# Kernel tuning notes

Hardware: AMD Instinct MI355X
Metric: run time of the kernel (lower is better)

## Reference

```python
import jax, jax.numpy as jnp
import numpy as np

OUT = 8192   # out_features
IN = 8192    # in_features
GS = 64      # HQQ group_size (axis=0 grouping)
NG = OUT * IN // GS   # number of quantization groups = 1048576
B = 64       # tokens in the batch


def setup_inputs() -> dict:
    key = jax.random.key(0)
    k1, k2, k3, k4, k5 = jax.random.split(key, 5)
    x = jax.random.normal(k1, (B, IN), dtype=jnp.float32)
    # packed 4-bit weights: two 4-bit values per byte, packed along axis 0
    # (HQQ pack_4bit_u8: packed = (W[:GS//2] << 4) | W[GS//2:])
    W_q = jax.random.randint(k2, (GS // 2, NG), 0, 256, dtype=jnp.int32)
    scale = jax.random.uniform(k3, (1, NG), dtype=jnp.float32, minval=0.001, maxval=0.02)
    zero = jax.random.uniform(k4, (1, NG), dtype=jnp.float32, minval=0.0, maxval=15.0)
    bias = jax.random.normal(k5, (OUT,), dtype=jnp.float32) * 0.01
    return {"x": x, "W_q": W_q, "scale": scale, "zero": zero, "bias": bias}


def reference(x, W_q, scale, zero, bias):
    # Unpack 4-bit: high nibble holds rows [0, GS//2), low nibble rows [GS//2, GS)
    hi = (W_q >> 4).astype(jnp.float32)          # (GS//2, NG)
    lo = (W_q & 0xF).astype(jnp.float32)         # (GS//2, NG)
    Wu = jnp.concatenate([hi, lo], axis=0)       # (GS, NG)
    # HQQ group-wise dequant: W = (W_q - zero) * scale, then reshape to (out, in)
    W = ((Wu - zero) * scale).reshape(OUT, IN)
    # linear: y = x @ W^T + bias
    return x @ W.T + bias
```

## Files before the change

### kernel.cpp

```cpp
#include <hip/hip_runtime.h>
#include <stdint.h>

#define OUT_F 8192
#define IN_F  8192
#define NGRP  1048576
#define BATCH 64
#define KS    2
#define NSTEP ((IN_F / KS) / 128)

typedef float f32x4 __attribute__((ext_vector_type(4)));
typedef _Float16 half8_t __attribute__((ext_vector_type(8)));

static __device__ __forceinline__ unsigned int pk_fma_f16(unsigned int a, unsigned int b, unsigned int c) {
  unsigned int d;
  asm("v_pk_fma_f16 %0, %1, %2, %3" : "=v"(d) : "v"(a), "v"(b), "v"(c));
  return d;
}
static __device__ __forceinline__ unsigned int pk16(float a, float b) {
  unsigned short ua = __builtin_bit_cast(unsigned short, (_Float16)a);
  unsigned short ub = __builtin_bit_cast(unsigned short, (_Float16)b);
  return (unsigned int)ua | ((unsigned int)ub << 16);
}

#define GLL16(g, l)                                                         \
  __builtin_amdgcn_global_load_lds(                                         \
      (const __attribute__((address_space(1))) void*)(g),                   \
      (__attribute__((address_space(3))) void*)(l), 16, 0, 0)

__global__ __launch_bounds__(256) void pre_kernel(const float* __restrict__ x, ushort* __restrict__ xh,
                                                  const float* __restrict__ scale, const float* __restrict__ zero,
                                                  uint32_t* __restrict__ szb) {
  const int b = blockIdx.x;
  if (b < 512) {
    const int i = b * 256 + threadIdx.x;
    float4 v = ((const float4*)x)[i];
    ushort4 o;
    o.x = __builtin_bit_cast(unsigned short, (_Float16)v.x);
    o.y = __builtin_bit_cast(unsigned short, (_Float16)v.y);
    o.z = __builtin_bit_cast(unsigned short, (_Float16)v.z);
    o.w = __builtin_bit_cast(unsigned short, (_Float16)v.w);
    ((ushort4*)xh)[i] = o;
  } else {
    const int i = (b - 512) * 256 + threadIdx.x;
    float4 s = ((const float4*)scale)[i];
    float4 z = ((const float4*)zero)[i];
    uint4 o;
    o.x = pk16(s.x, s.y);
    o.y = pk16(-(64.f + z.x) * s.x, -(64.f + z.y) * s.y);
    o.z = pk16(s.z, s.w);
    o.w = pk16(-(64.f + z.z) * s.z, -(64.f + z.w) * s.w);
    ((uint4*)szb)[i] = o;
  }
}

__global__ __launch_bounds__(256, 2) void hqq_gemm_kernel(
    const int* __restrict__ Wq, const uint32_t* __restrict__ szb,
    const ushort* __restrict__ xh, float* __restrict__ part)
{
  __shared__ ushort xlds[3][64 * 128];
  __shared__ ushort blds[2][32 * 128];

  const int t    = threadIdx.x;
  const int bid  = blockIdx.x;
  const int ks   = bid & 1;
  const int gq   = (bid >> 1) & 1;
  const int c    = bid >> 2;
  const int lane = t & 63;
  const int wid  = t >> 6;
  const int kbase = ks * (IN_F / KS);

  const int sr  = t >> 4;
  const int skq = t & 15;
  const int* __restrict__ wqp =
      Wq + (size_t)(gq * 16 + sr) * NGRP + (size_t)c * IN_F + kbase + skq * 8;
  const uint8_t* __restrict__ szp =
      (const uint8_t*)szb + ((size_t)c * IN_F + kbase + skq * 8) * 4;
  const int wbyte = (skq * 16) ^ ((sr & 7) << 4);

  const int tr    = lane & 15;
  const int koff8 = (lane >> 4) * 8;
  const int am    = wid * 16 + tr;

  f32x4 acc_h = {0.f, 0.f, 0.f, 0.f};
  f32x4 acc_l = {0.f, 0.f, 0.f, 0.f};

  auto stage_x = [&](int bi, int s) {
    #pragma unroll
    for (int j = 0; j < 4; ++j) {
      const int m    = wid * 16 + j * 4 + (lane >> 4);
      const int bcol = (lane & 15) * 16;
      const int scol = bcol ^ ((m & 7) << 4);
      const ushort* g = xh + (size_t)m * IN_F + kbase + s * 128 + (scol >> 1);
      ushort* l = &xlds[bi][(wid * 16 + j * 4) * 128];
      GLL16(g, l);
    }
  };

  auto ldregs = [&](int s, int4& wa, int4& wb, uint4& sa, uint4& sb) {
    wa = *(const int4*)(wqp + (size_t)s * 128);
    wb = *(const int4*)(wqp + (size_t)s * 128 + 4);
    sa = *(const uint4*)(szp + (size_t)s * 512);
    sb = *(const uint4*)(szp + (size_t)s * 512 + 16);
  };

  auto stage_b = [&](int bi, const int4& wa, const int4& wb, const uint4& sa, const uint4& sb) {
    uint8_t* bb = (uint8_t*)&blds[bi][0];
    uint4 hi4, lo4;
    {
      unsigned tt = ((unsigned)wa.y << 16) | (unsigned)wa.x;
      hi4.x = pk_fma_f16((tt & 0x00F000F0u) | 0x54005400u, sa.x, sa.y);
      lo4.x = pk_fma_f16(((tt << 4) & 0x00F000F0u) | 0x54005400u, sa.x, sa.y);
    }
    {
      unsigned tt = ((unsigned)wa.w << 16) | (unsigned)wa.z;
      hi4.y = pk_fma_f16((tt & 0x00F000F0u) | 0x54005400u, sa.z, sa.w);
      lo4.y = pk_fma_f16(((tt << 4) & 0x00F000F0u) | 0x54005400u, sa.z, sa.w);
    }
    {
      unsigned tt = ((unsigned)wb.y << 16) | (unsigned)wb.x;
      hi4.z = pk_fma_f16((tt & 0x00F000F0u) | 0x54005400u, sb.x, sb.y);
      lo4.z = pk_fma_f16(((tt << 4) & 0x00F000F0u) | 0x54005400u, sb.x, sb.y);
    }
    {
      unsigned tt = ((unsigned)wb.w << 16) | (unsigned)wb.z;
      hi4.w = pk_fma_f16((tt & 0x00F000F0u) | 0x54005400u, sb.z, sb.w);
      lo4.w = pk_fma_f16(((tt << 4) & 0x00F000F0u) | 0x54005400u, sb.z, sb.w);
    }
    *(uint4*)(bb + sr * 256 + wbyte)        = hi4;
    *(uint4*)(bb + (sr + 16) * 256 + wbyte) = lo4;
  };

  {
    int4 wa0, wb0; uint4 sa0, sb0;
    ldregs(0, wa0, wb0, sa0, sb0);
    stage_b(0, wa0, wb0, sa0, sb0);
  }
  stage_x(0, 0);
  stage_x(1, 1);
  int4 wa, wb; uint4 sa, sb;
  ldregs(1, wa, wb, sa, sb);

  int xr0 = 0, xr1 = 1, xr2 = 2;

  #pragma unroll 1
  for (int s = 0; s < NSTEP; ++s) {
    asm volatile("s_waitcnt lgkmcnt(0)" ::: "memory");
    __builtin_amdgcn_s_barrier();

    const bool more2 = (s + 2 < NSTEP);
    int4 nwa, nwb; uint4 nsa, nsb;
    if (more2) {
      stage_x(xr2, s + 2);
      ldregs(s + 2, nwa, nwb, nsa, nsb);
    }

    if (more2)               asm volatile("s_waitcnt vmcnt(16)" ::: "memory");
    else if (s + 1 < NSTEP)  asm volatile("s_waitcnt vmcnt(8)" ::: "memory");
    else                     asm volatile("s_waitcnt vmcnt(0)" ::: "memory");
    __builtin_amdgcn_sched_barrier(0);

    const uint8_t* xb = (const uint8_t*)&xlds[xr0][0];
    const uint8_t* bb = (const uint8_t*)&blds[s & 1][0];
    #pragma unroll
    for (int kk = 0; kk < 4; ++kk) {
      const int colb = (koff8 + kk * 32) * 2;
      half8_t a   = *(const half8_t*)(xb + am * 256 + (colb ^ ((am & 7) << 4)));
      half8_t bhi = *(const half8_t*)(bb + tr * 256 + (colb ^ ((tr & 7) << 4)));
      half8_t blo = *(const half8_t*)(bb + (tr + 16) * 256 + (colb ^ ((tr & 7) << 4)));
      acc_h = __builtin_amdgcn_mfma_f32_16x16x32_f16(a, bhi, acc_h, 0, 0, 0);
      acc_l = __builtin_amdgcn_mfma_f32_16x16x32_f16(a, blo, acc_l, 0, 0, 0);
    }

    if (s + 1 < NSTEP) stage_b((s + 1) & 1, wa, wb, sa, sb);
    if (more2) { wa = nwa; wb = nwb; sa = nsa; sb = nsb; }

    const int tmp = xr0; xr0 = xr1; xr1 = xr2; xr2 = tmp;
  }

  const int o_hi = (gq * 16 + tr) * 128 + c;
  const int m0   = wid * 16 + (lane >> 4) * 4;
  float* p_hi = part + ((size_t)ks * OUT_F + o_hi) * BATCH + m0;
  float* p_lo = part + ((size_t)ks * OUT_F + o_hi + 4096) * BATCH + m0;
  *(float4*)p_hi = (float4){acc_h[0], acc_h[1], acc_h[2], acc_h[3]};
  *(float4*)p_lo = (float4){acc_l[0], acc_l[1], acc_l[2], acc_l[3]};
}

__global__ __launch_bounds__(256) void reduce_kernel(const float* __restrict__ part,
                                                     const float* __restrict__ bias,
                                                     float* __restrict__ out)
{
  __shared__ float tile[32][65];
  const int ob = blockIdx.x;
  const int t  = threadIdx.x;
  {
    const int ol = t >> 3;
    const int mg = t & 7;
    const int o  = ob * 32 + ol;
    const size_t base = (size_t)o * BATCH + mg * 8;
    float s[8] = {0, 0, 0, 0, 0, 0, 0, 0};
    #pragma unroll
    for (int ks = 0; ks < KS; ++ks) {
      const float* p = part + (size_t)ks * OUT_F * BATCH + base;
      float4 a = *(const float4*)p;
      float4 b = *(const float4*)(p + 4);
      s[0] += a.x; s[1] += a.y; s[2] += a.z; s[3] += a.w;
      s[4] += b.x; s[5] += b.y; s[6] += b.z; s[7] += b.w;
    }
    const float bv = bias[o];
    #pragma unroll
    for (int j = 0; j < 8; ++j) tile[ol][mg * 8 + j] = s[j] + bv;
  }
  __syncthreads();
  {
    const int m  = t >> 2;
    const int og = (t & 3) * 8;
    float r[8];
    #pragma unroll
    for (int j = 0; j < 8; ++j) r[j] = tile[og + j][m];
    float* op = out + (size_t)m * OUT_F + ob * 32 + og;
    *(float4*)op       = (float4){r[0], r[1], r[2], r[3]};
    *(float4*)(op + 4) = (float4){r[4], r[5], r[6], r[7]};
  }
}

__global__ void hqq_fallback_kernel(const float* __restrict__ x, const int* __restrict__ Wq,
                                    const float* __restrict__ scale, const float* __restrict__ zero,
                                    const float* __restrict__ bias, float* __restrict__ out)
{
  int idx = blockIdx.x * blockDim.x + threadIdx.x;
  int b = idx >> 13;
  int o = idx & 8191;
  int g = o >> 7, cc = o & 127;
  int r = g & 31;
  bool hi = (g < 32);
  const int*   wrow = Wq    + (size_t)r  * NGRP + (size_t)cc * IN_F;
  const float* srow = scale + (size_t)cc * IN_F;
  const float* zrow = zero  + (size_t)cc * IN_F;
  const float* xrow = x     + (size_t)b  * IN_F;
  float acc = 0.f;
  for (int k = 0; k < IN_F; ++k) {
    int v = wrow[k];
    float nib = (float)(hi ? (v >> 4) : (v & 15));
    acc += xrow[k] * ((nib - zrow[k]) * srow[k]);
  }
  out[idx] = acc + bias[o];
}

extern "C" void kernel_launch(void* const* d_in, const int* in_sizes, int n_in,
                              void* d_out, int out_size, void* d_ws, size_t ws_size,
                              hipStream_t stream) {
  const float* x     = (const float*)d_in[0];
  const int*   Wq    = (const int*)d_in[1];
  const float* scale = (const float*)d_in[2];
  const float* zero  = (const float*)d_in[3];
  const float* bias  = (const float*)d_in[4];
  float* out = (float*)d_out;

  const size_t xh_bytes   = (size_t)BATCH * IN_F * sizeof(ushort);
  const size_t sz_bytes   = (size_t)NGRP * 4;
  const size_t part_bytes = (size_t)KS * BATCH * OUT_F * sizeof(float);

  if (ws_size >= xh_bytes + sz_bytes + part_bytes) {
    ushort*   xh   = (ushort*)d_ws;
    uint32_t* szb  = (uint32_t*)((char*)d_ws + xh_bytes);
    float*    part = (float*)((char*)d_ws + xh_bytes + sz_bytes);
    pre_kernel<<<1536, 256, 0, stream>>>(x, xh, scale, zero, szb);
    hqq_gemm_kernel<<<128 * 2 * KS, 256, 0, stream>>>(Wq, szb, xh, part);
    reduce_kernel<<<OUT_F / 32, 256, 0, stream>>>(part, bias, out);
  } else {
    hqq_fallback_kernel<<<(BATCH * OUT_F) / 256, 256, 0, stream>>>(x, Wq, scale, zero, bias, out);
  }
}
```

Before: 47.05 us.

## Load activations directly to registers, split K four ways, deepen weight prefetch

Drops the LDS staging buffer for activations, so each lane loads its MFMA A-fragments straight from global memory into registers, double-buffered. The K split goes from 2 to 4 to launch more blocks, and occupancy is raised to 4 blocks per CU. Weight and scale prefetch becomes three-deep in registers, and the step loop is fully unrolled. The aim is to cut LDS traffic and footprint and to hide latency with more parallelism. In exchange there are more partial sums for the reduce kernel, more register pressure, and duplicated x reads across waves.

```diff
diff --git a/kernel.cpp b/kernel.cpp
--- a/kernel.cpp
+++ b/kernel.cpp
@@ -5,7 +5,7 @@
 #define IN_F  8192
 #define NGRP  1048576
 #define BATCH 64
-#define KS    2
+#define KS    4
 #define NSTEP ((IN_F / KS) / 128)
 
 typedef float f32x4 __attribute__((ext_vector_type(4)));
@@ -21,11 +21,6 @@
   unsigned short ub = __builtin_bit_cast(unsigned short, (_Float16)b);
   return (unsigned int)ua | ((unsigned int)ub << 16);
 }
-
-#define GLL16(g, l)                                                         \
-  __builtin_amdgcn_global_load_lds(                                         \
-      (const __attribute__((address_space(1))) void*)(g),                   \
-      (__attribute__((address_space(3))) void*)(l), 16, 0, 0)
 
 __global__ __launch_bounds__(256) void pre_kernel(const float* __restrict__ x, ushort* __restrict__ xh,
                                                   const float* __restrict__ scale, const float* __restrict__ zero,
@@ -53,18 +48,17 @@
   }
 }
 
-__global__ __launch_bounds__(256, 2) void hqq_gemm_kernel(
+__global__ __launch_bounds__(256, 4) void hqq_gemm_kernel(
     const int* __restrict__ Wq, const uint32_t* __restrict__ szb,
     const ushort* __restrict__ xh, float* __restrict__ part)
 {
-  __shared__ ushort xlds[3][64 * 128];
   __shared__ ushort blds[2][32 * 128];
 
   const int t    = threadIdx.x;
   const int bid  = blockIdx.x;
-  const int ks   = bid & 1;
-  const int gq   = (bid >> 1) & 1;
-  const int c    = bid >> 2;
+  const int ks   = bid & 3;
+  const int gq   = (bid >> 2) & 1;
+  const int c    = bid >> 3;
   const int lane = t & 63;
   const int wid  = t >> 6;
   const int kbase = ks * (IN_F / KS);
@@ -80,102 +74,91 @@
   const int tr    = lane & 15;
   const int koff8 = (lane >> 4) * 8;
   const int am    = wid * 16 + tr;
+  const ushort* __restrict__ xrow = xh + (size_t)am * IN_F + kbase + koff8;
 
   f32x4 acc_h = {0.f, 0.f, 0.f, 0.f};
   f32x4 acc_l = {0.f, 0.f, 0.f, 0.f};
 
-  auto stage_x = [&](int bi, int s) {
-    #pragma unroll
-    for (int j = 0; j < 4; ++j) {
-      const int m    = wid * 16 + j * 4 + (lane >> 4);
-      const int bcol = (lane & 15) * 16;
-      const int scol = bcol ^ ((m & 7) << 4);
-      const ushort* g = xh + (size_t)m * IN_F + kbase + s * 128 + (scol >> 1);
-      ushort* l = &xlds[bi][(wid * 16 + j * 4) * 128];
-      GLL16(g, l);
-    }
-  };
-
-  auto ldregs = [&](int s, int4& wa, int4& wb, uint4& sa, uint4& sb) {
-    wa = *(const int4*)(wqp + (size_t)s * 128);
-    wb = *(const int4*)(wqp + (size_t)s * 128 + 4);
-    sa = *(const uint4*)(szp + (size_t)s * 512);
-    sb = *(const uint4*)(szp + (size_t)s * 512 + 16);
-  };
-
-  auto stage_b = [&](int bi, const int4& wa, const int4& wb, const uint4& sa, const uint4& sb) {
+  int4  wa[3], wb[3];
+  uint4 sa[3], sb[3];
+  half8_t areg[2][4];
+
+  #define LDW(set, s)                                                \
+    do {                                                             \
+      wa[set] = *(const int4*)(wqp + (size_t)(s) * 128);             \
+      wb[set] = *(const int4*)(wqp + (size_t)(s) * 128 + 4);         \
+      sa[set] = *(const uint4*)(szp + (size_t)(s) * 512);            \
+      sb[set] = *(const uint4*)(szp + (size_t)(s) * 512 + 16);       \
+    } while (0)
+  #define LDA(set, s)                                                \
+    do {                                                             \
+      _Pragma("unroll")                                              \
+      for (int kk = 0; kk < 4; ++kk)                                 \
+        areg[set][kk] = *(const half8_t*)(xrow + (s) * 128 + kk * 32); \
+    } while (0)
+
+  auto stage_b = [&](int bi, const int4& Wa, const int4& Wb, const uint4& Sa, const uint4& Sb) {
     uint8_t* bb = (uint8_t*)&blds[bi][0];
     uint4 hi4, lo4;
     {
-      unsigned tt = ((unsigned)wa.y << 16) | (unsigned)wa.x;
-      hi4.x = pk_fma_f16((tt & 0x00F000F0u) | 0x54005400u, sa.x, sa.y);
-      lo4.x = pk_fma_f16(((tt << 4) & 0x00F000F0u) | 0x54005400u, sa.x, sa.y);
-    }
-    {
-      unsigned tt = ((unsigned)wa.w << 16) | (unsigned)wa.z;
-      hi4.y = pk_fma_f16((tt & 0x00F000F0u) | 0x54005400u, sa.z, sa.w);
-      lo4.y = pk_fma_f16(((tt << 4) & 0x00F000F0u) | 0x54005400u, sa.z, sa.w);
-    }
-    {
-      unsigned tt = ((unsigned)wb.y << 16) | (unsigned)wb.x;
-      hi4.z = pk_fma_f16((tt & 0x00F000F0u) | 0x54005400u, sb.x, sb.y);
-      lo4.z = pk_fma_f16(((tt << 4) & 0x00F000F0u) | 0x54005400u, sb.x, sb.y);
-    }
-    {
-      unsigned tt = ((unsigned)wb.w << 16) | (unsigned)wb.z;
-      hi4.w = pk_fma_f16((tt & 0x00F000F0u) | 0x54005400u, sb.z, sb.w);
-      lo4.w = pk_fma_f16(((tt << 4) & 0x00F000F0u) | 0x54005400u, sb.z, sb.w);
+      unsigned tt = ((unsigned)Wa.y << 16) | (unsigned)Wa.x;
+      hi4.x = pk_fma_f16((tt & 0x00F000F0u) | 0x54005400u, Sa.x, Sa.y);
+      lo4.x = pk_fma_f16(((tt << 4) & 0x00F000F0u) | 0x54005400u, Sa.x, Sa.y);
+    }
+    {
+      unsigned tt = ((unsigned)Wa.w << 16) | (unsigned)Wa.z;
+      hi4.y = pk_fma_f16((tt & 0x00F000F0u) | 0x54005400u, Sa.z, Sa.w);
+      lo4.y = pk_fma_f16(((tt << 4) & 0x00F000F0u) | 0x54005400u, Sa.z, Sa.w);
+    }
+    {
+      unsigned tt = ((unsigned)Wb.y << 16) | (unsigned)Wb.x;
+      hi4.z = pk_fma_f16((tt & 0x00F000F0u) | 0x54005400u, Sb.x, Sb.y);
+      lo4.z = pk_fma_f16(((tt << 4) & 0x00F000F0u) | 0x54005400u, Sb.x, Sb.y);
+    }
+    {
+      unsigned tt = ((unsigned)Wb.w << 16) | (unsigned)Wb.z;
+      hi4.w = pk_fma_f16((tt & 0x00F000F0u) | 0x54005400u, Sb.z, Sb.w);
+      lo4.w = pk_fma_f16(((tt << 4) & 0x00F000F0u) | 0x54005400u, Sb.z, Sb.w);
     }
     *(uint4*)(bb + sr * 256 + wbyte)        = hi4;
     *(uint4*)(bb + (sr + 16) * 256 + wbyte) = lo4;
   };
 
-  {
-    int4 wa0, wb0; uint4 sa0, sb0;
-    ldregs(0, wa0, wb0, sa0, sb0);
-    stage_b(0, wa0, wb0, sa0, sb0);
-  }
-  stage_x(0, 0);
-  stage_x(1, 1);
-  int4 wa, wb; uint4 sa, sb;
-  ldregs(1, wa, wb, sa, sb);
-
-  int xr0 = 0, xr1 = 1, xr2 = 2;
-
-  #pragma unroll 1
+  LDW(0, 0);
+  LDW(1, 1);
+  LDW(2, 2);
+  LDA(0, 0);
+  LDA(1, 1);
+  stage_b(0, wa[0], wb[0], sa[0], sb[0]);
+  asm volatile("s_waitcnt lgkmcnt(0)" ::: "memory");
+  __builtin_amdgcn_s_barrier();
+
+  #pragma unroll
   for (int s = 0; s < NSTEP; ++s) {
-    asm volatile("s_waitcnt lgkmcnt(0)" ::: "memory");
-    __builtin_amdgcn_s_barrier();
-
-    const bool more2 = (s + 2 < NSTEP);
-    int4 nwa, nwb; uint4 nsa, nsb;
-    if (more2) {
-      stage_x(xr2, s + 2);
-      ldregs(s + 2, nwa, nwb, nsa, nsb);
-    }
-
-    if (more2)               asm volatile("s_waitcnt vmcnt(16)" ::: "memory");
-    else if (s + 1 < NSTEP)  asm volatile("s_waitcnt vmcnt(8)" ::: "memory");
-    else                     asm volatile("s_waitcnt vmcnt(0)" ::: "memory");
-    __builtin_amdgcn_sched_barrier(0);
-
-    const uint8_t* xb = (const uint8_t*)&xlds[xr0][0];
     const uint8_t* bb = (const uint8_t*)&blds[s & 1][0];
     #pragma unroll
     for (int kk = 0; kk < 4; ++kk) {
       const int colb = (koff8 + kk * 32) * 2;
-      half8_t a   = *(const half8_t*)(xb + am * 256 + (colb ^ ((am & 7) << 4)));
+      half8_t a   = areg[s & 1][kk];
       half8_t bhi = *(const half8_t*)(bb + tr * 256 + (colb ^ ((tr & 7) << 4)));
       half8_t blo = *(const half8_t*)(bb + (tr + 16) * 256 + (colb ^ ((tr & 7) << 4)));
       acc_h = __builtin_amdgcn_mfma_f32_16x16x32_f16(a, bhi, acc_h, 0, 0, 0);
       acc_l = __builtin_amdgcn_mfma_f32_16x16x32_f16(a, blo, acc_l, 0, 0, 0);
     }
 
-    if (s + 1 < NSTEP) stage_b((s + 1) & 1, wa, wb, sa, sb);
-    if (more2) { wa = nwa; wb = nwb; sa = nsa; sb = nsb; }
-
-    const int tmp = xr0; xr0 = xr1; xr1 = xr2; xr2 = tmp;
-  }
+    if (s + 1 < NSTEP)
+      stage_b((s + 1) & 1, wa[(s + 1) % 3], wb[(s + 1) % 3], sa[(s + 1) % 3], sb[(s + 1) % 3]);
+
+    if (s + 2 < NSTEP) LDA(s & 1, s + 2);
+    if (s + 3 < NSTEP) LDW(s % 3, s + 3);
+
+    if (s + 1 < NSTEP) {
+      asm volatile("s_waitcnt lgkmcnt(0)" ::: "memory");
+      __builtin_amdgcn_s_barrier();
+    }
+  }
+  #undef LDW
+  #undef LDA
 
   const int o_hi = (gq * 16 + tr) * 128 + c;
   const int m0   = wid * 16 + (lane >> 4) * 4;
```

New measurement: 52.67 us. 1.12x slower.

## Stage packed weights and scales to LDS asynchronously and dequantize at MFMA time

Applied to the files above, without the earlier changes.

Packed int4 weights and fp16 scale/offset pairs now go straight into LDS through global_load_lds with a 4-deep ring. Each wave dequantizes its own MFMA B fragments from LDS inside the compute loop, so the register staging and the separate dequant-then-store round trip are gone. The K-split rises from 2 to 4 to launch more blocks, and the x buffer drops from triple to double buffering. The cost is a larger partial-sum buffer for the reduce kernel, repeated dequant work across waves, and a small pad in the workspace layout.

```diff
diff --git a/kernel.cpp b/kernel.cpp
--- a/kernel.cpp
+++ b/kernel.cpp
@@ -5,7 +5,7 @@
 #define IN_F  8192
 #define NGRP  1048576
 #define BATCH 64
-#define KS    2
+#define KS    4
 #define NSTEP ((IN_F / KS) / 128)
 
 typedef float f32x4 __attribute__((ext_vector_type(4)));
@@ -57,29 +57,31 @@
     const int* __restrict__ Wq, const uint32_t* __restrict__ szb,
     const ushort* __restrict__ xh, float* __restrict__ part)
 {
-  __shared__ ushort xlds[3][64 * 128];
-  __shared__ ushort blds[2][32 * 128];
+  __shared__ ushort   xlds[2][64 * 128];
+  __shared__ unsigned wlds[4][16 * 128];
+  __shared__ unsigned szlds[4][256];
 
   const int t    = threadIdx.x;
   const int bid  = blockIdx.x;
-  const int ks   = bid & 1;
-  const int gq   = (bid >> 1) & 1;
-  const int c    = bid >> 2;
+  const int ks   = bid & 3;
+  const int gq   = (bid >> 2) & 1;
+  const int c    = bid >> 3;
   const int lane = t & 63;
   const int wid  = t >> 6;
   const int kbase = ks * (IN_F / KS);
 
-  const int sr  = t >> 4;
-  const int skq = t & 15;
-  const int* __restrict__ wqp =
-      Wq + (size_t)(gq * 16 + sr) * NGRP + (size_t)c * IN_F + kbase + skq * 8;
-  const uint8_t* __restrict__ szp =
-      (const uint8_t*)szb + ((size_t)c * IN_F + kbase + skq * 8) * 4;
-  const int wbyte = (skq * 16) ^ ((sr & 7) << 4);
-
-  const int tr    = lane & 15;
-  const int koff8 = (lane >> 4) * 8;
-  const int am    = wid * 16 + tr;
+  const int rt0 = wid * 4 + (lane >> 5);
+  const int rt1 = rt0 + 2;
+  const int* __restrict__ wsrc0 =
+      Wq + (size_t)(gq * 16 + rt0) * NGRP + (size_t)c * IN_F + kbase + ((lane & 31) ^ rt0) * 4;
+  const int* __restrict__ wsrc1 =
+      Wq + (size_t)(gq * 16 + rt1) * NGRP + (size_t)c * IN_F + kbase + ((lane & 31) ^ rt1) * 4;
+  const uint8_t* __restrict__ szsrc =
+      (const uint8_t*)szb + ((size_t)c * IN_F + kbase) * 4 + lane * 16;
+
+  const int tr = lane & 15;
+  const int l4 = lane >> 4;
+  const int am = wid * 16 + tr;
 
   f32x4 acc_h = {0.f, 0.f, 0.f, 0.f};
   f32x4 acc_l = {0.f, 0.f, 0.f, 0.f};
@@ -88,97 +90,76 @@
     #pragma unroll
     for (int j = 0; j < 4; ++j) {
       const int m    = wid * 16 + j * 4 + (lane >> 4);
-      const int bcol = (lane & 15) * 16;
-      const int scol = bcol ^ ((m & 7) << 4);
+      const int scol = ((lane & 15) * 16) ^ ((m & 7) << 4);
       const ushort* g = xh + (size_t)m * IN_F + kbase + s * 128 + (scol >> 1);
-      ushort* l = &xlds[bi][(wid * 16 + j * 4) * 128];
-      GLL16(g, l);
+      GLL16(g, &xlds[bi][(wid * 16 + j * 4) * 128]);
     }
   };
-
-  auto ldregs = [&](int s, int4& wa, int4& wb, uint4& sa, uint4& sb) {
-    wa = *(const int4*)(wqp + (size_t)s * 128);
-    wb = *(const int4*)(wqp + (size_t)s * 128 + 4);
-    sa = *(const uint4*)(szp + (size_t)s * 512);
-    sb = *(const uint4*)(szp + (size_t)s * 512 + 16);
+  auto stage_wsz = [&](int bi, int s) {
+    GLL16(wsrc0 + (size_t)s * 128, &wlds[bi][(wid * 4) * 128]);
+    GLL16(wsrc1 + (size_t)s * 128, &wlds[bi][(wid * 4 + 2) * 128]);
+    GLL16(szsrc + (size_t)s * 512, &szlds[bi][0]);
   };
 
-  auto stage_b = [&](int bi, const int4& wa, const int4& wb, const uint4& sa, const uint4& sb) {
-    uint8_t* bb = (uint8_t*)&blds[bi][0];
-    uint4 hi4, lo4;
-    {
-      unsigned tt = ((unsigned)wa.y << 16) | (unsigned)wa.x;
-      hi4.x = pk_fma_f16((tt & 0x00F000F0u) | 0x54005400u, sa.x, sa.y);
-      lo4.x = pk_fma_f16(((tt << 4) & 0x00F000F0u) | 0x54005400u, sa.x, sa.y);
-    }
-    {
-      unsigned tt = ((unsigned)wa.w << 16) | (unsigned)wa.z;
-      hi4.y = pk_fma_f16((tt & 0x00F000F0u) | 0x54005400u, sa.z, sa.w);
-      lo4.y = pk_fma_f16(((tt << 4) & 0x00F000F0u) | 0x54005400u, sa.z, sa.w);
-    }
-    {
-      unsigned tt = ((unsigned)wb.y << 16) | (unsigned)wb.x;
-      hi4.z = pk_fma_f16((tt & 0x00F000F0u) | 0x54005400u, sb.x, sb.y);
-      lo4.z = pk_fma_f16(((tt << 4) & 0x00F000F0u) | 0x54005400u, sb.x, sb.y);
-    }
-    {
-      unsigned tt = ((unsigned)wb.w << 16) | (unsigned)wb.z;
-      hi4.w = pk_fma_f16((tt & 0x00F000F0u) | 0x54005400u, sb.z, sb.w);
-      lo4.w = pk_fma_f16(((tt << 4) & 0x00F000F0u) | 0x54005400u, sb.z, sb.w);
-    }
-    *(uint4*)(bb + sr * 256 + wbyte)        = hi4;
-    *(uint4*)(bb + (sr + 16) * 256 + wbyte) = lo4;
-  };
-
-  {
-    int4 wa0, wb0; uint4 sa0, sb0;
-    ldregs(0, wa0, wb0, sa0, sb0);
-    stage_b(0, wa0, wb0, sa0, sb0);
-  }
   stage_x(0, 0);
-  stage_x(1, 1);
-  int4 wa, wb; uint4 sa, sb;
-  ldregs(1, wa, wb, sa, sb);
-
-  int xr0 = 0, xr1 = 1, xr2 = 2;
+  stage_wsz(0, 0);
+  stage_wsz(1, 1);
 
   #pragma unroll 1
   for (int s = 0; s < NSTEP; ++s) {
-    asm volatile("s_waitcnt lgkmcnt(0)" ::: "memory");
+    if (s + 1 < NSTEP) stage_x((s + 1) & 1, s + 1);
+    if (s + 2 < NSTEP) stage_wsz((s + 2) & 3, s + 2);
+
+    if (s + 2 < NSTEP)      asm volatile("s_waitcnt vmcnt(10)" ::: "memory");
+    else if (s + 1 < NSTEP) asm volatile("s_waitcnt vmcnt(7)" ::: "memory");
+    else                    asm volatile("s_waitcnt vmcnt(0)" ::: "memory");
+    __builtin_amdgcn_sched_barrier(0);
     __builtin_amdgcn_s_barrier();
-
-    const bool more2 = (s + 2 < NSTEP);
-    int4 nwa, nwb; uint4 nsa, nsb;
-    if (more2) {
-      stage_x(xr2, s + 2);
-      ldregs(s + 2, nwa, nwb, nsa, nsb);
+    __builtin_amdgcn_sched_barrier(0);
+
+    const uint8_t* xb = (const uint8_t*)&xlds[s & 1][0];
+    const uint8_t* wb = (const uint8_t*)&wlds[s & 3][0];
+    const uint8_t* zb = (const uint8_t*)&szlds[s & 3][0];
+
+    #pragma unroll
+    for (int kk = 0; kk < 4; ++kk) {
+      const int o2 = (kk * 4 + l4) * 2;
+      uint4 q0 = *(const uint4*)(wb + tr * 512 + ((o2 ^ tr) << 4));
+      uint4 q1 = *(const uint4*)(wb + tr * 512 + (((o2 + 1) ^ tr) << 4));
+      uint4 sa = *(const uint4*)(zb + kk * 128 + l4 * 32);
+      uint4 sb = *(const uint4*)(zb + kk * 128 + l4 * 32 + 16);
+
+      union { uint4 u; half8_t h; } uh, ul;
+      {
+        unsigned tt = ((unsigned)q0.y << 16) | (unsigned)q0.x;
+        uh.u.x = pk_fma_f16((tt & 0x00F000F0u) | 0x54005400u, sa.x, sa.y);
+        ul.u.x = pk_fma_f16(((tt << 4) & 0x00F000F0u) | 0x54005400u, sa.x, sa.y);
+      }
+      {
+        unsigned tt = ((unsigned)q0.w << 16) | (unsigned)q0.z;
+        uh.u.y = pk_fma_f16((tt & 0x00F000F0u) | 0x54005400u, sa.z, sa.w);
+        ul.u.y = pk_fma_f16(((tt << 4) & 0x00F000F0u) | 0x54005400u, sa.z, sa.w);
+      }
+      {
+        unsigned tt = ((unsigned)q1.y << 16) | (unsigned)q1.x;
+        uh.u.z = pk_fma_f16((tt & 0x00F000F0u) | 0x54005400u, sb.x, sb.y);
+        ul.u.z = pk_fma_f16(((tt << 4) & 0x00F000F0u) | 0x54005400u, sb.x, sb.y);
+      }
+      {
+        unsigned tt = ((unsigned)q1.w << 16) | (unsigned)q1.z;
+        uh.u.w = pk_fma_f16((tt & 0x00F000F0u) | 0x54005400u, sb.z, sb.w);
+        ul.u.w = pk_fma_f16(((tt << 4) & 0x00F000F0u) | 0x54005400u, sb.z, sb.w);
+      }
+
+      const int colb = (l4 * 8 + kk * 32) * 2;
+      half8_t a = *(const half8_t*)(xb + am * 256 + (colb ^ ((am & 7) << 4)));
+      acc_h = __builtin_amdgcn_mfma_f32_16x16x32_f16(a, uh.h, acc_h, 0, 0, 0);
+      acc_l = __builtin_amdgcn_mfma_f32_16x16x32_f16(a, ul.h, acc_l, 0, 0, 0);
     }
-
-    if (more2)               asm volatile("s_waitcnt vmcnt(16)" ::: "memory");
-    else if (s + 1 < NSTEP)  asm volatile("s_waitcnt vmcnt(8)" ::: "memory");
-    else                     asm volatile("s_waitcnt vmcnt(0)" ::: "memory");
-    __builtin_amdgcn_sched_barrier(0);
-
-    const uint8_t* xb = (const uint8_t*)&xlds[xr0][0];
-    const uint8_t* bb = (const uint8_t*)&blds[s & 1][0];
-    #pragma unroll
-    for (int kk = 0; kk < 4; ++kk) {
-      const int colb = (koff8 + kk * 32) * 2;
-      half8_t a   = *(const half8_t*)(xb + am * 256 + (colb ^ ((am & 7) << 4)));
-      half8_t bhi = *(const half8_t*)(bb + tr * 256 + (colb ^ ((tr & 7) << 4)));
-      half8_t blo = *(const half8_t*)(bb + (tr + 16) * 256 + (colb ^ ((tr & 7) << 4)));
-      acc_h = __builtin_amdgcn_mfma_f32_16x16x32_f16(a, bhi, acc_h, 0, 0, 0);
-      acc_l = __builtin_amdgcn_mfma_f32_16x16x32_f16(a, blo, acc_l, 0, 0, 0);
-    }
-
-    if (s + 1 < NSTEP) stage_b((s + 1) & 1, wa, wb, sa, sb);
-    if (more2) { wa = nwa; wb = nwb; sa = nsa; sb = nsb; }
-
-    const int tmp = xr0; xr0 = xr1; xr1 = xr2; xr2 = tmp;
   }
 
   const int o_hi = (gq * 16 + tr) * 128 + c;
-  const int m0   = wid * 16 + (lane >> 4) * 4;
+  const int m0   = wid * 16 + l4 * 4;
   float* p_hi = part + ((size_t)ks * OUT_F + o_hi) * BATCH + m0;
   float* p_lo = part + ((size_t)ks * OUT_F + o_hi + 4096) * BATCH + m0;
   *(float4*)p_hi = (float4){acc_h[0], acc_h[1], acc_h[2], acc_h[3]};
@@ -259,11 +240,12 @@
   const size_t xh_bytes   = (size_t)BATCH * IN_F * sizeof(ushort);
   const size_t sz_bytes   = (size_t)NGRP * 4;
   const size_t part_bytes = (size_t)KS * BATCH * OUT_F * sizeof(float);
-
-  if (ws_size >= xh_bytes + sz_bytes + part_bytes) {
+  const size_t pad_bytes  = 1024;
+
+  if (ws_size >= xh_bytes + sz_bytes + part_bytes + pad_bytes) {
     ushort*   xh   = (ushort*)d_ws;
     uint32_t* szb  = (uint32_t*)((char*)d_ws + xh_bytes);
-    float*    part = (float*)((char*)d_ws + xh_bytes + sz_bytes);
+    float*    part = (float*)((char*)d_ws + xh_bytes + sz_bytes + pad_bytes);
     pre_kernel<<<1536, 256, 0, stream>>>(x, xh, scale, zero, szb);
     hqq_gemm_kernel<<<128 * 2 * KS, 256, 0, stream>>>(Wq, szb, xh, part);
     reduce_kernel<<<OUT_F / 32, 256, 0, stream>>>(part, bias, out);
```

New measurement: 55.14 us. 1.17x slower.

## Widen GEMM block to all 32 packed rows and split K four ways

Applied to the files above, without the earlier changes.

Each block now dequantizes all 32 packed weight rows (64 output columns) instead of half, so every x tile staged in LDS is reused across four MFMA accumulators rather than two. The K dimension is split four ways instead of two, keeping the grid at 512 blocks. Per-thread loads change to four row-strided int4 loads plus one scale/zero load. This halves redundant x staging and scale/zero loads per output, at the cost of more LDS per block, twice the partial-sum traffic for the reduce kernel, and different weight-load coalescing.

```diff
diff --git a/kernel.cpp b/kernel.cpp
--- a/kernel.cpp
+++ b/kernel.cpp
@@ -5,7 +5,7 @@
 #define IN_F  8192
 #define NGRP  1048576
 #define BATCH 64
-#define KS    2
+#define KS    4
 #define NSTEP ((IN_F / KS) / 128)
 
 typedef float f32x4 __attribute__((ext_vector_type(4)));
@@ -58,87 +58,82 @@
     const ushort* __restrict__ xh, float* __restrict__ part)
 {
   __shared__ ushort xlds[3][64 * 128];
-  __shared__ ushort blds[2][32 * 128];
+  __shared__ ushort blds[2][64 * 128];
 
   const int t    = threadIdx.x;
   const int bid  = blockIdx.x;
-  const int ks   = bid & 1;
-  const int gq   = (bid >> 1) & 1;
+  const int ks   = bid & 3;
   const int c    = bid >> 2;
   const int lane = t & 63;
   const int wid  = t >> 6;
   const int kbase = ks * (IN_F / KS);
 
-  const int sr  = t >> 4;
-  const int skq = t & 15;
-  const int* __restrict__ wqp =
-      Wq + (size_t)(gq * 16 + sr) * NGRP + (size_t)c * IN_F + kbase + skq * 8;
+  const int lr = t >> 5;
+  const int i0 = (t & 31) * 4;
+  const int* __restrict__ wq0 = Wq + (size_t)lr * NGRP + (size_t)c * IN_F + kbase + i0;
+  const int* __restrict__ wq1 = wq0 + (size_t)8 * NGRP;
+  const int* __restrict__ wq2 = wq0 + (size_t)16 * NGRP;
+  const int* __restrict__ wq3 = wq0 + (size_t)24 * NGRP;
   const uint8_t* __restrict__ szp =
-      (const uint8_t*)szb + ((size_t)c * IN_F + kbase + skq * 8) * 4;
-  const int wbyte = (skq * 16) ^ ((sr & 7) << 4);
+      (const uint8_t*)szb + ((size_t)c * IN_F + kbase + i0) * 4;
+  const int wb0 = (i0 * 2) ^ ((lr & 7) << 4);
 
   const int tr    = lane & 15;
   const int koff8 = (lane >> 4) * 8;
   const int am    = wid * 16 + tr;
 
-  f32x4 acc_h = {0.f, 0.f, 0.f, 0.f};
-  f32x4 acc_l = {0.f, 0.f, 0.f, 0.f};
+  f32x4 acc0 = {0.f, 0.f, 0.f, 0.f};
+  f32x4 acc1 = {0.f, 0.f, 0.f, 0.f};
+  f32x4 acc2 = {0.f, 0.f, 0.f, 0.f};
+  f32x4 acc3 = {0.f, 0.f, 0.f, 0.f};
 
   auto stage_x = [&](int bi, int s) {
     #pragma unroll
     for (int j = 0; j < 4; ++j) {
       const int m    = wid * 16 + j * 4 + (lane >> 4);
-      const int bcol = (lane & 15) * 16;
-      const int scol = bcol ^ ((m & 7) << 4);
+      const int scol = ((lane & 15) * 16) ^ ((m & 7) << 4);
       const ushort* g = xh + (size_t)m * IN_F + kbase + s * 128 + (scol >> 1);
-      ushort* l = &xlds[bi][(wid * 16 + j * 4) * 128];
-      GLL16(g, l);
+      GLL16(g, &xlds[bi][(wid * 16 + j * 4) * 128]);
     }
   };
 
-  auto ldregs = [&](int s, int4& wa, int4& wb, uint4& sa, uint4& sb) {
-    wa = *(const int4*)(wqp + (size_t)s * 128);
-    wb = *(const int4*)(wqp + (size_t)s * 128 + 4);
-    sa = *(const uint4*)(szp + (size_t)s * 512);
-    sb = *(const uint4*)(szp + (size_t)s * 512 + 16);
+  auto ldregs = [&](int s, int4& w0, int4& w1, int4& w2, int4& w3, uint4& z4) {
+    w0 = *(const int4*)(wq0 + (size_t)s * 128);
+    w1 = *(const int4*)(wq1 + (size_t)s * 128);
+    w2 = *(const int4*)(wq2 + (size_t)s * 128);
+    w3 = *(const int4*)(wq3 + (size_t)s * 128);
+    z4 = *(const uint4*)(szp + (size_t)s * 512);
   };
 
-  auto stage_b = [&](int bi, const int4& wa, const int4& wb, const uint4& sa, const uint4& sb) {
+  auto stage_b = [&](int bi, const int4& w0, const int4& w1, const int4& w2, const int4& w3,
+                     const uint4& z4) {
     uint8_t* bb = (uint8_t*)&blds[bi][0];
-    uint4 hi4, lo4;
-    {
-      unsigned tt = ((unsigned)wa.y << 16) | (unsigned)wa.x;
-      hi4.x = pk_fma_f16((tt & 0x00F000F0u) | 0x54005400u, sa.x, sa.y);
-      lo4.x = pk_fma_f16(((tt << 4) & 0x00F000F0u) | 0x54005400u, sa.x, sa.y);
-    }
-    {
-      unsigned tt = ((unsigned)wa.w << 16) | (unsigned)wa.z;
-      hi4.y = pk_fma_f16((tt & 0x00F000F0u) | 0x54005400u, sa.z, sa.w);
-      lo4.y = pk_fma_f16(((tt << 4) & 0x00F000F0u) | 0x54005400u, sa.z, sa.w);
-    }
-    {
-      unsigned tt = ((unsigned)wb.y << 16) | (unsigned)wb.x;
-      hi4.z = pk_fma_f16((tt & 0x00F000F0u) | 0x54005400u, sb.x, sb.y);
-      lo4.z = pk_fma_f16(((tt << 4) & 0x00F000F0u) | 0x54005400u, sb.x, sb.y);
-    }
-    {
-      unsigned tt = ((unsigned)wb.w << 16) | (unsigned)wb.z;
-      hi4.w = pk_fma_f16((tt & 0x00F000F0u) | 0x54005400u, sb.z, sb.w);
-      lo4.w = pk_fma_f16(((tt << 4) & 0x00F000F0u) | 0x54005400u, sb.z, sb.w);
-    }
-    *(uint4*)(bb + sr * 256 + wbyte)        = hi4;
-    *(uint4*)(bb + (sr + 16) * 256 + wbyte) = lo4;
+    auto dqrow = [&](const int4& wv, int r) {
+      unsigned tt0 = ((unsigned)wv.y << 16) | (unsigned)wv.x;
+      unsigned tt1 = ((unsigned)wv.w << 16) | (unsigned)wv.z;
+      uint2 hh, ll;
+      hh.x = pk_fma_f16((tt0 & 0x00F000F0u) | 0x54005400u, z4.x, z4.y);
+      hh.y = pk_fma_f16((tt1 & 0x00F000F0u) | 0x54005400u, z4.z, z4.w);
+      ll.x = pk_fma_f16(((tt0 << 4) & 0x00F000F0u) | 0x54005400u, z4.x, z4.y);
+      ll.y = pk_fma_f16(((tt1 << 4) & 0x00F000F0u) | 0x54005400u, z4.z, z4.w);
+      *(uint2*)(bb + r * 256 + wb0)        = hh;
+      *(uint2*)(bb + (r + 32) * 256 + wb0) = ll;
+    };
+    dqrow(w0, lr);
+    dqrow(w1, lr + 8);
+    dqrow(w2, lr + 16);
+    dqrow(w3, lr + 24);
   };
 
   {
-    int4 wa0, wb0; uint4 sa0, sb0;
-    ldregs(0, wa0, wb0, sa0, sb0);
-    stage_b(0, wa0, wb0, sa0, sb0);
+    int4 a0, a1, a2, a3; uint4 z0;
+    ldregs(0, a0, a1, a2, a3, z0);
+    stage_b(0, a0, a1, a2, a3, z0);
   }
   stage_x(0, 0);
   stage_x(1, 1);
-  int4 wa, wb; uint4 sa, sb;
-  ldregs(1, wa, wb, sa, sb);
+  int4 w0, w1, w2, w3; uint4 z4;
+  ldregs(1, w0, w1, w2, w3, z4);
 
   int xr0 = 0, xr1 = 1, xr2 = 2;
 
@@ -148,41 +143,46 @@
     __builtin_amdgcn_s_barrier();
 
     const bool more2 = (s + 2 < NSTEP);
-    int4 nwa, nwb; uint4 nsa, nsb;
+    int4 n0, n1, n2, n3; uint4 nz;
     if (more2) {
       stage_x(xr2, s + 2);
-      ldregs(s + 2, nwa, nwb, nsa, nsb);
-    }
-
-    if (more2)               asm volatile("s_waitcnt vmcnt(16)" ::: "memory");
-    else if (s + 1 < NSTEP)  asm volatile("s_waitcnt vmcnt(8)" ::: "memory");
+      ldregs(s + 2, n0, n1, n2, n3, nz);
+    }
+
+    if (more2)               asm volatile("s_waitcnt vmcnt(18)" ::: "memory");
+    else if (s + 1 < NSTEP)  asm volatile("s_waitcnt vmcnt(9)" ::: "memory");
     else                     asm volatile("s_waitcnt vmcnt(0)" ::: "memory");
     __builtin_amdgcn_sched_barrier(0);
 
     const uint8_t* xb = (const uint8_t*)&xlds[xr0][0];
-    const uint8_t* bb = (const uint8_t*)&blds[s & 1][0];
+    const uint8_t* bbuf = (const uint8_t*)&blds[s & 1][0];
     #pragma unroll
     for (int kk = 0; kk < 4; ++kk) {
       const int colb = (koff8 + kk * 32) * 2;
-      half8_t a   = *(const half8_t*)(xb + am * 256 + (colb ^ ((am & 7) << 4)));
-      half8_t bhi = *(const half8_t*)(bb + tr * 256 + (colb ^ ((tr & 7) << 4)));
-      half8_t blo = *(const half8_t*)(bb + (tr + 16) * 256 + (colb ^ ((tr & 7) << 4)));
-      acc_h = __builtin_amdgcn_mfma_f32_16x16x32_f16(a, bhi, acc_h, 0, 0, 0);
-      acc_l = __builtin_amdgcn_mfma_f32_16x16x32_f16(a, blo, acc_l, 0, 0, 0);
-    }
-
-    if (s + 1 < NSTEP) stage_b((s + 1) & 1, wa, wb, sa, sb);
-    if (more2) { wa = nwa; wb = nwb; sa = nsa; sb = nsb; }
+      const int bcol = colb ^ ((tr & 7) << 4);
+      half8_t a  = *(const half8_t*)(xb + am * 256 + (colb ^ ((am & 7) << 4)));
+      half8_t b0 = *(const half8_t*)(bbuf + tr * 256 + bcol);
+      half8_t b1 = *(const half8_t*)(bbuf + (tr + 16) * 256 + bcol);
+      half8_t b2 = *(const half8_t*)(bbuf + (tr + 32) * 256 + bcol);
+      half8_t b3 = *(const half8_t*)(bbuf + (tr + 48) * 256 + bcol);
+      acc0 = __builtin_amdgcn_mfma_f32_16x16x32_f16(a, b0, acc0, 0, 0, 0);
+      acc1 = __builtin_amdgcn_mfma_f32_16x16x32_f16(a, b1, acc1, 0, 0, 0);
+      acc2 = __builtin_amdgcn_mfma_f32_16x16x32_f16(a, b2, acc2, 0, 0, 0);
+      acc3 = __builtin_amdgcn_mfma_f32_16x16x32_f16(a, b3, acc3, 0, 0, 0);
+    }
+
+    if (s + 1 < NSTEP) stage_b((s + 1) & 1, w0, w1, w2, w3, z4);
+    if (more2) { w0 = n0; w1 = n1; w2 = n2; w3 = n3; z4 = nz; }
 
     const int tmp = xr0; xr0 = xr1; xr1 = xr2; xr2 = tmp;
   }
 
-  const int o_hi = (gq * 16 + tr) * 128 + c;
-  const int m0   = wid * 16 + (lane >> 4) * 4;
-  float* p_hi = part + ((size_t)ks * OUT_F + o_hi) * BATCH + m0;
-  float* p_lo = part + ((size_t)ks * OUT_F + o_hi + 4096) * BATCH + m0;
-  *(float4*)p_hi = (float4){acc_h[0], acc_h[1], acc_h[2], acc_h[3]};
-  *(float4*)p_lo = (float4){acc_l[0], acc_l[1], acc_l[2], acc_l[3]};
+  const int m0 = wid * 16 + (lane >> 4) * 4;
+  float* base = part + (size_t)ks * OUT_F * BATCH + (size_t)m0;
+  *(float4*)(base + (size_t)(tr * 128 + c) * BATCH)        = (float4){acc0[0], acc0[1], acc0[2], acc0[3]};
+  *(float4*)(base + (size_t)((tr + 16) * 128 + c) * BATCH) = (float4){acc1[0], acc1[1], acc1[2], acc1[3]};
+  *(float4*)(base + (size_t)((tr + 32) * 128 + c) * BATCH) = (float4){acc2[0], acc2[1], acc2[2], acc2[3]};
+  *(float4*)(base + (size_t)((tr + 48) * 128 + c) * BATCH) = (float4){acc3[0], acc3[1], acc3[2], acc3[3]};
 }
 
 __global__ __launch_bounds__(256) void reduce_kernel(const float* __restrict__ part,
@@ -265,7 +265,7 @@
     uint32_t* szb  = (uint32_t*)((char*)d_ws + xh_bytes);
     float*    part = (float*)((char*)d_ws + xh_bytes + sz_bytes);
     pre_kernel<<<1536, 256, 0, stream>>>(x, xh, scale, zero, szb);
-    hqq_gemm_kernel<<<128 * 2 * KS, 256, 0, stream>>>(Wq, szb, xh, part);
+    hqq_gemm_kernel<<<128 * KS, 256, 0, stream>>>(Wq, szb, xh, part);
     reduce_kernel<<<OUT_F / 32, 256, 0, stream>>>(part, bias, out);
   } else {
     hqq_fallback_kernel<<<(BATCH * OUT_F) / 256, 256, 0, stream>>>(x, Wq, scale, zero, bias, out);
```

After: 42.15 us. 1.12x faster.
